# Kernel tuning notes

Measured on AMD Instinct MI355X. Metric: run time of the kernel, lower is better.

The kernel has to match this reference:

```python
import jax, jax.numpy as jnp
import numpy as np

N_HEAD = 12
HEAD_DIM = 64
EPS = 1e-6
ROPE_BASE = 10000.0


def rms_norm(x, w):
    x32 = x.astype(jnp.float32)
    var = jnp.mean(x32 * x32, axis=-1, keepdims=True)
    xn = x32 * jax.lax.rsqrt(var + EPS)
    return w * xn.astype(x.dtype)


def rotate_half(x):
    x1, x2 = jnp.split(x, 2, axis=-1)
    return jnp.concatenate((-x2, x1), axis=-1)


def rope_cos_sin(seq_len, dtype):
    inv_freq = 1.0 / (ROPE_BASE ** (jnp.arange(0, HEAD_DIM, 2, dtype=jnp.float32) / HEAD_DIM))
    pos = jnp.arange(seq_len, dtype=jnp.float32)
    freqs = pos[:, None] * inv_freq[None, :]          # [S, HEAD_DIM//2]
    emb = jnp.concatenate((freqs, freqs), axis=-1)    # [S, HEAD_DIM]
    # shape [1, 1, S, HEAD_DIM] (batch, head, seq, dim) after unsqueeze_dim=1
    return emb[None, None].astype(dtype), None  # placeholder, see below


def setup_inputs() -> dict:
    key = jax.random.key(0)
    ks = jax.random.split(key, 9)
    B, S, D, F = 1, 4096, 768, 2048
    s = 0.02
    return {
        "hidden_states": jax.random.normal(ks[0], (B, S, D), jnp.float32),
        "w_q": jax.random.normal(ks[1], (D, D), jnp.float32) * s,
        "w_k": jax.random.normal(ks[2], (D, D), jnp.float32) * s,
        "w_v": jax.random.normal(ks[3], (D, D), jnp.float32) * s,
        "w_o": jax.random.normal(ks[4], (D, D), jnp.float32) * s,
        "w_gate": jax.random.normal(ks[5], (D, F), jnp.float32) * s,
        "w_up": jax.random.normal(ks[6], (D, F), jnp.float32) * s,
        "w_down": jax.random.normal(ks[7], (F, D), jnp.float32) * s,
        "w_norm1": jnp.ones((D,), jnp.float32),
        "w_norm2": jnp.ones((D,), jnp.float32),
    }


def attention(x, w_q, w_k, w_v, w_o):
    B, S, D = x.shape
    scale = HEAD_DIM ** -0.5
    # project and split heads: [B, H, S, hd]
    q = (x @ w_q).reshape(B, S, N_HEAD, HEAD_DIM).transpose(0, 2, 1, 3)
    k = (x @ w_k).reshape(B, S, N_HEAD, HEAD_DIM).transpose(0, 2, 1, 3)
    v = (x @ w_v).reshape(B, S, N_HEAD, HEAD_DIM).transpose(0, 2, 1, 3)
    # rotary embedding (position_ids = arange(S))
    inv_freq = 1.0 / (ROPE_BASE ** (jnp.arange(0, HEAD_DIM, 2, dtype=jnp.float32) / HEAD_DIM))
    pos = jnp.arange(S, dtype=jnp.float32)
    freqs = pos[:, None] * inv_freq[None, :]
    emb = jnp.concatenate((freqs, freqs), axis=-1)          # [S, hd]
    cos = jnp.cos(emb).astype(x.dtype)[None, None]          # [1,1,S,hd]
    sin = jnp.sin(emb).astype(x.dtype)[None, None]
    q = q * cos + rotate_half(q) * sin
    k = k * cos + rotate_half(k) * sin
    # eager attention with causal mask (materialized, as in the original)
    scores = jnp.einsum("bhqd,bhkd->bhqk", q, k) * scale
    causal = jnp.triu(jnp.ones((S, S), dtype=bool), k=1)
    scores = jnp.where(causal, jnp.finfo(scores.dtype).min, scores)
    attn = jax.nn.softmax(scores.astype(jnp.float32), axis=-1).astype(q.dtype)
    out = jnp.einsum("bhqk,bhkd->bhqd", attn, v)
    out = out.transpose(0, 2, 1, 3).reshape(B, S, D)
    return out @ w_o


def reference(hidden_states, w_q, w_k, w_v, w_o, w_gate, w_up, w_down, w_norm1, w_norm2):
    x = hidden_states
    h = x + attention(rms_norm(x, w_norm1), w_q, w_k, w_v, w_o)
    y = rms_norm(h, w_norm2)
    ffn = (jax.nn.silu(y @ w_gate) * (y @ w_up)) @ w_down
    return h + ffn
```

## Files before the change

kernel.cpp:

```cpp
#include <hip/hip_runtime.h>
#include <hip/hip_bf16.h>

typedef __attribute__((ext_vector_type(8))) short s8v;
typedef __attribute__((ext_vector_type(4))) float f4v;
typedef __attribute__((ext_vector_type(16))) float f16v;
typedef __attribute__((ext_vector_type(4))) unsigned u4v;

typedef __attribute__((address_space(1))) const void as1_void;
typedef __attribute__((address_space(3))) void as3_void;

__device__ __forceinline__ void gl16(const void* g, void* l) {
  __builtin_amdgcn_global_load_lds((as1_void*)g, (as3_void*)l, 16, 0, 0);
}

__device__ __forceinline__ float b2f(int u) {
  union { float f; unsigned i; } c; c.i = ((unsigned)(u & 0xFFFF)) << 16; return c.f;
}
__device__ __forceinline__ unsigned short f2b(float f) {
  union { float f; unsigned i; } c; c.f = f;
  unsigned r = c.i + 0x7FFFu + ((c.i >> 16) & 1u);
  return (unsigned short)(r >> 16);
}
__device__ __forceinline__ unsigned pk2(float lo, float hi) {
  unsigned u;
  asm("v_cvt_pk_bf16_f32 %0, %1, %2" : "=v"(u) : "v"(lo), "v"(hi));
  return u;
}

#define MFMA16(a, b, c) __builtin_amdgcn_mfma_f32_16x16x32_bf16((a), (b), (c), 0, 0, 0)
#define MFMA32(a, b, c) __builtin_amdgcn_mfma_f32_32x32x16_bf16((a), (b), (c), 0, 0, 0)

__device__ __forceinline__ void xcd_remap(int nbn, int& bm, int& bn) {
  const int flat = blockIdx.x;
  const int u = (flat & 7) * ((int)gridDim.x >> 3) + (flat >> 3);
  bm = u / nbn;
  bn = u - bm * nbn;
}

struct Seg { const float* src; unsigned short* dst; int K; int N; int nbn; int nblocks; int mode; };
struct PrepArgs { Seg seg[9]; float* ct; float* st; const float* wn1; };

__global__ __launch_bounds__(256) void prep_k(PrepArgs a) {
  int b = blockIdx.x, si = 0;
  while (si < 8 && b >= a.seg[si].nblocks) { b -= a.seg[si].nblocks; ++si; }
  const Seg s = a.seg[si];
  const int tid = threadIdx.x;
  if (s.mode == 3) {
    const int t = b * 256 + tid;
    const int sq = t >> 5, d = t & 31;
    const float inv = powf(10000.0f, -(float)d * (1.0f / 32.0f));
    const float ang = (float)sq * inv;
    a.ct[t] = cosf(ang);
    a.st[t] = sinf(ang);
    return;
  }
  if (s.mode == 4) {
    const float* xr = s.src + (size_t)b * 768;
    float v0 = xr[tid], v1 = xr[tid + 256], v2 = xr[tid + 512];
    float ss = v0 * v0 + v1 * v1 + v2 * v2;
#pragma unroll
    for (int m = 1; m < 64; m <<= 1) ss += __shfl_xor(ss, m, 64);
    __shared__ float sred[4];
    if ((tid & 63) == 0) sred[tid >> 6] = ss;
    __syncthreads();
    const float tot = sred[0] + sred[1] + sred[2] + sred[3];
    const float rn = rsqrtf(tot * (1.0f / 768.0f) + 1e-6f);
    unsigned short* orow = s.dst + (size_t)b * 768;
    orow[tid]       = f2b(v0 * rn * a.wn1[tid]);
    orow[tid + 256] = f2b(v1 * rn * a.wn1[tid + 256]);
    orow[tid + 512] = f2b(v2 * rn * a.wn1[tid + 512]);
    return;
  }
  __shared__ float tile[32][33];
  const int tx = tid & 31, ty = tid >> 5;
  const int bn = b % s.nbn, bk = b / s.nbn;
#pragma unroll
  for (int i = 0; i < 32; i += 8)
    tile[ty + i][tx] = s.src[(size_t)(bk * 32 + ty + i) * s.N + bn * 32 + tx];
  __syncthreads();
#pragma unroll
  for (int i = 0; i < 32; i += 8) {
    int row;
    if (s.mode == 0)      row = bn * 32 + ty + i;
    else                  row = bn * 64 + (s.mode == 2 ? 32 : 0) + ty + i;
    s.dst[(size_t)row * s.K + bk * 32 + tx] = f2b(tile[tx][ty + i]);
  }
}

__global__ __launch_bounds__(256) void rmsnorm_k(const float* __restrict__ x,
    const float* __restrict__ w, unsigned short* __restrict__ out) {
  const int row = blockIdx.x, tid = threadIdx.x;
  const float* xr = x + (size_t)row * 768;
  float v0 = xr[tid], v1 = xr[tid + 256], v2 = xr[tid + 512];
  float ss = v0 * v0 + v1 * v1 + v2 * v2;
#pragma unroll
  for (int m = 1; m < 64; m <<= 1) ss += __shfl_xor(ss, m, 64);
  __shared__ float sred[4];
  if ((tid & 63) == 0) sred[tid >> 6] = ss;
  __syncthreads();
  const float tot = sred[0] + sred[1] + sred[2] + sred[3];
  const float rn = rsqrtf(tot * (1.0f / 768.0f) + 1e-6f);
  unsigned short* orow = out + (size_t)row * 768;
  orow[tid]       = f2b(v0 * rn * w[tid]);
  orow[tid + 256] = f2b(v1 * rn * w[tid + 256]);
  orow[tid + 512] = f2b(v2 * rn * w[tid + 512]);
}

template <int EPI, int BM, int BN>
__global__ __launch_bounds__(256) void gemm_bt(const unsigned short* __restrict__ A,
    const unsigned short* __restrict__ Bt, unsigned short* __restrict__ Cb,
    float* __restrict__ Cf, const float* __restrict__ R, int K, int ldc,
    const float* __restrict__ ct, const float* __restrict__ st, int nbn) {
  constexpr int ABYTES = BM * 32 * 2;
  constexpr int BBYTES = BN * 32 * 2;
  constexpr int APASS = BM / 64, BPASS = BN / 64;
  constexpr int LPS = APASS + BPASS;
  constexpr int MR = (BM == 128 && BN == 128) ? 4 : (BM == 128 ? 2 : 1);
  __shared__ unsigned short As[3 * BM * 32];
  __shared__ unsigned short Bs[3 * BN * 32];
  const int tid = threadIdx.x;
  const int lane = tid & 63, wid = tid >> 6;
  const int wrow = (BN == 128) ? (wid >> 1) * 64 : wid * (BM / 4);
  const int wcol = (BN == 128) ? (wid & 1) * 64 : 0;
  const int l15 = lane & 15, l4 = lane >> 4;
  int bm, bn;
  xcd_remap(nbn, bm, bn);

  f4v acc[MR][4] = {};

  const int o0 = tid * 16, o1 = tid * 16 + 4096;
  const int r0 = o0 >> 6, c0 = o0 & 63;
  const int r1 = o1 >> 6, c1 = o1 & 63;
  const size_t ldab = (size_t)K * 2;
  const char* Abyte = (const char*)A;
  const char* Bbyte = (const char*)Bt;
  const size_t a0 = (size_t)(bm * BM + r0) * ldab + c0;
  const size_t a1 = (size_t)(bm * BM + (APASS == 2 ? r1 : r0)) * ldab + c1;
  const size_t b0 = (size_t)(bn * BN + r0) * ldab + c0;
  const size_t b1 = (size_t)(bn * BN + (BPASS == 2 ? r1 : r0)) * ldab + c1;
  char* AsB = (char*)As;
  char* BsB = (char*)Bs;
  const int uoff = wid << 10;

#define STAGEK(I, SL) do { const size_t kb = (size_t)(I) * 64;                 \
    char* Aw = AsB + (SL) * ABYTES;                                            \
    char* Bw = BsB + (SL) * BBYTES;                                            \
    gl16(Abyte + a0 + kb, Aw + uoff);                                          \
    if constexpr (APASS == 2) gl16(Abyte + a1 + kb, Aw + uoff + 4096);         \
    gl16(Bbyte + b0 + kb, Bw + uoff);                                          \
    if constexpr (BPASS == 2) gl16(Bbyte + b1 + kb, Bw + uoff + 4096); } while (0)

  const int NI = K >> 5;
  STAGEK(0, 0);
  STAGEK(1, 1);
  int sel = 0, nsl = 2;

  for (int i = 0; i < NI; ++i) {
    if (i < NI - 1) {
      if constexpr (LPS == 4)      asm volatile("s_waitcnt vmcnt(4)" ::: "memory");
      else if constexpr (LPS == 3) asm volatile("s_waitcnt vmcnt(3)" ::: "memory");
      else                         asm volatile("s_waitcnt vmcnt(2)" ::: "memory");
    } else {
      asm volatile("s_waitcnt vmcnt(0)" ::: "memory");
    }
    __builtin_amdgcn_s_barrier();
    __builtin_amdgcn_sched_barrier(0);
    if (i + 2 < NI) STAGEK(i + 2, nsl);
    const char* Ar = AsB + sel * ABYTES;
    const char* Br = BsB + sel * BBYTES;
    s8v af[MR], bf[4];
#pragma unroll
    for (int m = 0; m < MR; ++m)
      af[m] = *(const s8v*)(Ar + (wrow + m * 16 + l15) * 64 + l4 * 16);
#pragma unroll
    for (int n = 0; n < 4; ++n)
      bf[n] = *(const s8v*)(Br + (wcol + n * 16 + l15) * 64 + l4 * 16);
    __builtin_amdgcn_s_setprio(1);
#pragma unroll
    for (int m = 0; m < MR; ++m)
#pragma unroll
      for (int n = 0; n < 4; ++n) acc[m][n] = MFMA16(af[m], bf[n], acc[m][n]);
    __builtin_amdgcn_s_setprio(0);
    sel = (sel == 2) ? 0 : sel + 1;
    nsl = (nsl == 2) ? 0 : nsl + 1;
  }
#undef STAGEK

  const int row0 = bm * BM + wrow;
  const int col0 = bn * BN + wcol;

  if constexpr (EPI == 2) {
    if (bn < 12) {
#pragma unroll
      for (int m = 0; m < MR; ++m)
#pragma unroll
        for (int r = 0; r < 4; ++r) {
          const int row = row0 + m * 16 + l4 * 4 + r;
#pragma unroll
          for (int n = 0; n < 2; ++n) {
            const int d = n * 16 + l15;
            const float c  = ct[row * 32 + d];
            const float sn = st[row * 32 + d];
            const float aa = acc[m][n][r], bb = acc[m][n + 2][r];
            acc[m][n][r]     = aa * c - bb * sn;
            acc[m][n + 2][r] = bb * c + aa * sn;
          }
        }
    }
    if (bn < 6) {
      const float QSC = 0.18033688011112042f;
#pragma unroll
      for (int m = 0; m < MR; ++m)
#pragma unroll
        for (int n = 0; n < 4; ++n)
#pragma unroll
          for (int r = 0; r < 4; ++r) acc[m][n][r] *= QSC;
    }
  }

#pragma unroll
  for (int m = 0; m < MR; ++m)
#pragma unroll
    for (int n = 0; n < 4; ++n)
#pragma unroll
      for (int r = 0; r < 4; ++r) {
        const int row = row0 + m * 16 + l4 * 4 + r;
        const int col = col0 + n * 16 + l15;
        const float v = acc[m][n][r];
        if (EPI == 1) {
          Cf[(size_t)row * ldc + col] = v + R[(size_t)row * ldc + col];
        } else {
          Cb[(size_t)row * ldc + col] = f2b(v);
        }
      }
}

template <int EPI>
__global__ __launch_bounds__(512, 2) void gemm_big(const unsigned short* __restrict__ A,
    const unsigned short* __restrict__ Bt, unsigned short* __restrict__ Cb,
    int K, int ldc, int nbn) {
  constexpr int ABYTES = 256 * 32 * 2;
  constexpr int BBYTES = 128 * 32 * 2;
  __shared__ unsigned short As[3 * 256 * 32];
  __shared__ unsigned short Bs[3 * 128 * 32];
  const int tid = threadIdx.x;
  const int lane = tid & 63, wid = tid >> 6;
  const int wm = wid >> 1, wn = wid & 1;
  const int wrow = wm * 64, wcol = wn * 64;
  const int l15 = lane & 15, l4 = lane >> 4;
  int bm, bn;
  xcd_remap(nbn, bm, bn);

  f4v acc[4][4] = {};

  const size_t ldab = (size_t)K * 2;
  const char* Ab = (const char*)A;
  const char* Bb = (const char*)Bt;
  const int lrow = lane >> 2, lch = (lane & 3) * 16;
  const size_t aS0 = (size_t)(bm * 256 + wid * 16 + lrow) * ldab + lch;
  const size_t aS1 = (size_t)(bm * 256 + (wid + 8) * 16 + lrow) * ldab + lch;
  const size_t bS  = (size_t)(bn * 128 + wid * 16 + lrow) * ldab + lch;
  char* AsB = (char*)As;
  char* BsB = (char*)Bs;
  const int uA0 = wid << 10, uA1 = (wid + 8) << 10, uB = wid << 10;

#define STAGEK(I, SL) do { const size_t kb = (size_t)(I) * 64;                 \
    gl16(Ab + aS0 + kb, AsB + (SL) * ABYTES + uA0);                            \
    gl16(Ab + aS1 + kb, AsB + (SL) * ABYTES + uA1);                            \
    gl16(Bb + bS  + kb, BsB + (SL) * BBYTES + uB); } while (0)

  const int NI = K >> 5;
  STAGEK(0, 0);
  STAGEK(1, 1);
  int sel = 0, nsl = 2;

  for (int i = 0; i < NI; ++i) {
    if (i < NI - 1) asm volatile("s_waitcnt vmcnt(3)" ::: "memory");
    else            asm volatile("s_waitcnt vmcnt(0)" ::: "memory");
    __builtin_amdgcn_s_barrier();
    __builtin_amdgcn_sched_barrier(0);
    if (i + 2 < NI) STAGEK(i + 2, nsl);
    const char* Ar = AsB + sel * ABYTES;
    const char* Br = BsB + sel * BBYTES;
    s8v af[4], bf[4];
#pragma unroll
    for (int m = 0; m < 4; ++m)
      af[m] = *(const s8v*)(Ar + (wrow + m * 16 + l15) * 64 + l4 * 16);
#pragma unroll
    for (int n = 0; n < 4; ++n)
      bf[n] = *(const s8v*)(Br + (wcol + n * 16 + l15) * 64 + l4 * 16);
    __builtin_amdgcn_s_setprio(1);
#pragma unroll
    for (int m = 0; m < 4; ++m)
#pragma unroll
      for (int n = 0; n < 4; ++n) acc[m][n] = MFMA16(af[m], bf[n], acc[m][n]);
    __builtin_amdgcn_s_setprio(0);
    sel = (sel == 2) ? 0 : sel + 1;
    nsl = (nsl == 2) ? 0 : nsl + 1;
  }
#undef STAGEK

  const int row0 = bm * 256 + wrow;
  const int col0 = bn * 128 + wcol;

  if (EPI == 3) {
    const int colb = (bn * 2 + wn) * 32;
#pragma unroll
    for (int m = 0; m < 4; ++m)
#pragma unroll
      for (int n = 0; n < 2; ++n)
#pragma unroll
        for (int r = 0; r < 4; ++r) {
          const int row = row0 + m * 16 + l4 * 4 + r;
          const float g = acc[m][n][r], u = acc[m][n + 2][r];
          const float val = g * u / (1.0f + __expf(-g));
          Cb[(size_t)row * 2048 + colb + n * 16 + l15] = f2b(val);
        }
    return;
  }

#pragma unroll
  for (int m = 0; m < 4; ++m)
#pragma unroll
    for (int n = 0; n < 4; ++n)
#pragma unroll
      for (int r = 0; r < 4; ++r) {
        const int row = row0 + m * 16 + l4 * 4 + r;
        const int col = col0 + n * 16 + l15;
        Cb[(size_t)row * ldc + col] = f2b(acc[m][n][r]);
      }
}

__global__ __launch_bounds__(256, 4) void flash_k(const unsigned short* __restrict__ qkv,
    uint2* __restrict__ Opart, float* __restrict__ ml) {
  const int kh = blockIdx.x, p = blockIdx.y, h = blockIdx.z;
  const int qbA = 63 - p;
  const int tid = threadIdx.x;
  const int wv = tid >> 6, lane = tid & 63;
  const int l31 = lane & 31, h8 = lane >> 5;
  const int myqb = (wv & 1) ? p : qbA;
  const int qrel = (wv >> 1) * 32 + l31;
  const int q_abs = myqb * 64 + qrel;

  __shared__ unsigned short Ks[2][64 * 72];
  __shared__ unsigned short Vt[2][64 * 72];

  const unsigned short* qp = qkv + h * 64;
  const unsigned short* kp = qkv + 768 + h * 64;
  const unsigned short* vp = qkv + 1536 + h * 64;

  s8v qf[4];
#pragma unroll
  for (int cc = 0; cc < 4; ++cc)
    qf[cc] = *(const s8v*)(qp + (size_t)q_abs * 2304 + cc * 16 + h8 * 8);

  f16v o0 = {}, o1 = {};
  float lp = 0.f;

  const int krow = tid >> 3, kc = (tid & 7) * 8;
  const int vj = tid & 31, vd0 = (tid >> 5) * 8;

  s8v ka, kb, va, vb;
#define LOADT(T) do { const size_t k0n = (size_t)(T) * 64;                    \
    ka = *(const s8v*)(kp + (k0n + krow) * 2304 + kc);                        \
    kb = *(const s8v*)(kp + (k0n + krow + 32) * 2304 + kc);                   \
    va = *(const s8v*)(vp + (k0n + 2 * vj) * 2304 + vd0);                     \
    vb = *(const s8v*)(vp + (k0n + 2 * vj + 1) * 2304 + vd0); } while (0)
#define WRITET(BUF) do {                                                      \
    *(s8v*)(Ks[BUF] + krow * 72 + kc) = ka;                                   \
    *(s8v*)(Ks[BUF] + (krow + 32) * 72 + kc) = kb;                            \
    unsigned* vtw = (unsigned*)(Vt[BUF] + (size_t)vd0 * 72 + 2 * vj);         \
    _Pragma("unroll")                                                         \
    for (int i = 0; i < 8; ++i)                                               \
      vtw[i * 36] = ((unsigned)(unsigned short)va[i]) |                       \
                    (((unsigned)(unsigned short)vb[i]) << 16); } while (0)

  LOADT(kh);
  WRITET(0);
  if (kh + 2 <= qbA) LOADT(kh + 2);
  __syncthreads();

  for (int t = kh; t <= qbA; t += 2) {
    const int cur = (t >> 1) & 1;
    if (t <= myqb) {
      f16v s0 = {}, s1 = {};
      __builtin_amdgcn_s_setprio(1);
#pragma unroll
      for (int cc = 0; cc < 4; ++cc) {
        const s8v kf0 = *(const s8v*)(Ks[cur] + l31 * 72 + cc * 16 + h8 * 8);
        const s8v kf1 = *(const s8v*)(Ks[cur] + (32 + l31) * 72 + cc * 16 + h8 * 8);
        s0 = MFMA32(kf0, qf[cc], s0);
        s1 = MFMA32(kf1, qf[cc], s1);
      }
      __builtin_amdgcn_s_setprio(0);
      if (t == myqb) {
#pragma unroll
        for (int rr = 0; rr < 16; ++rr) {
          const int koff = (rr & 3) + 8 * (rr >> 2) + 4 * h8;
          if (koff > qrel) s0[rr] = -1e30f;
          if (koff + 32 > qrel) s1[rr] = -1e30f;
        }
      }
#pragma unroll
      for (int rr = 0; rr < 16; ++rr) {
        s0[rr] = exp2f(s0[rr]);
        s1[rr] = exp2f(s1[rr]);
      }
      float sm[8];
#pragma unroll
      for (int i = 0; i < 8; ++i) sm[i] = (s0[i] + s0[i + 8]) + (s1[i] + s1[i + 8]);
#pragma unroll
      for (int i = 0; i < 4; ++i) sm[i] += sm[i + 4];
      lp += (sm[0] + sm[1]) + (sm[2] + sm[3]);

      unsigned pk0[8], pk1[8];
#pragma unroll
      for (int g = 0; g < 4; ++g)
#pragma unroll
        for (int j = 0; j < 2; ++j) {
          pk0[g * 2 + j] = pk2(s0[g * 4 + 2 * j], s0[g * 4 + 2 * j + 1]);
          pk1[g * 2 + j] = pk2(s1[g * 4 + 2 * j], s1[g * 4 + 2 * j + 1]);
        }
      __builtin_amdgcn_s_setprio(1);
#pragma unroll
      for (int cc = 0; cc < 4; ++cc) {
        const int g0 = (cc & 1) * 2, g1 = g0 + 1;
        const unsigned pA0 = (cc & 2) ? pk1[g0 * 2 + 0] : pk0[g0 * 2 + 0];
        const unsigned pA1 = (cc & 2) ? pk1[g0 * 2 + 1] : pk0[g0 * 2 + 1];
        const unsigned pB0 = (cc & 2) ? pk1[g1 * 2 + 0] : pk0[g1 * 2 + 0];
        const unsigned pB1 = (cc & 2) ? pk1[g1 * 2 + 1] : pk0[g1 * 2 + 1];
        const unsigned t00 = __shfl_xor((int)pA0, 32);
        const unsigned t01 = __shfl_xor((int)pA1, 32);
        const unsigned t10 = __shfl_xor((int)pB0, 32);
        const unsigned t11 = __shfl_xor((int)pB1, 32);
        union { u4v u; s8v s; } pf;
        pf.u[0] = h8 ? t10 : pA0;
        pf.u[1] = h8 ? t11 : pA1;
        pf.u[2] = h8 ? pB0 : t00;
        pf.u[3] = h8 ? pB1 : t01;
        const s8v vf0 = *(const s8v*)(Vt[cur] + l31 * 72 + cc * 16 + h8 * 8);
        const s8v vf1 = *(const s8v*)(Vt[cur] + (32 + l31) * 72 + cc * 16 + h8 * 8);
        o0 = MFMA32(vf0, pf.s, o0);
        o1 = MFMA32(vf1, pf.s, o1);
      }
      __builtin_amdgcn_s_setprio(0);
    }
    if (t + 2 <= qbA) {
      WRITET(cur ^ 1);
      if (t + 4 <= qbA) LOADT(t + 4);
      __syncthreads();
    }
  }

  lp += __shfl_xor(lp, 32);

  const size_t obase = ((size_t)kh * 12 + h) * 16 * 4096;
#pragma unroll
  for (int g = 0; g < 4; ++g) {
    const uint2 v0 = make_uint2(pk2(o0[g * 4], o0[g * 4 + 1]), pk2(o0[g * 4 + 2], o0[g * 4 + 3]));
    const uint2 v1 = make_uint2(pk2(o1[g * 4], o1[g * 4 + 1]), pk2(o1[g * 4 + 2], o1[g * 4 + 3]));
    Opart[obase + (size_t)(2 * g + h8) * 4096 + q_abs] = v0;
    Opart[obase + (size_t)(8 + 2 * g + h8) * 4096 + q_abs] = v1;
  }
  if (h8 == 0)
    ml[((size_t)kh * 12 + h) * 4096 + q_abs] = lp;
#undef LOADT
#undef WRITET
}

__global__ __launch_bounds__(256) void combine_k(const uint2* __restrict__ Opart,
    const float* __restrict__ ml, unsigned short* __restrict__ out) {
  const int u = blockIdx.x * 256 + threadIdx.x;
  const int q = u & 4095;
  const int rest = u >> 12;
  const int dgrp = rest & 15;
  const int h = rest >> 4;
  const float l0 = ml[h * 4096 + q];
  const float l1 = ml[12 * 4096 + h * 4096 + q];
  const float inv = 1.0f / (l0 + l1);
  const size_t idx = ((size_t)h * 16 + dgrp) * 4096 + q;
  const uint2 a = Opart[idx];
  const uint2 b = Opart[(size_t)12 * 16 * 4096 + idx];
  const int dbase = (dgrp < 8) ? 4 * dgrp : 32 + 4 * (dgrp - 8);
  ushort4 r;
  r.x = f2b((b2f(a.x) + b2f(b.x)) * inv);
  r.y = f2b((b2f(a.x >> 16) + b2f(b.x >> 16)) * inv);
  r.z = f2b((b2f(a.y) + b2f(b.y)) * inv);
  r.w = f2b((b2f(a.y >> 16) + b2f(b.y >> 16)) * inv);
  *(ushort4*)(out + (size_t)q * 768 + h * 64 + dbase) = r;
}

extern "C" void kernel_launch(void* const* d_in, const int* in_sizes, int n_in,
                              void* d_out, int out_size, void* d_ws, size_t ws_size,
                              hipStream_t stream) {
  const float* x    = (const float*)d_in[0];
  const float* w_q  = (const float*)d_in[1];
  const float* w_k  = (const float*)d_in[2];
  const float* w_v  = (const float*)d_in[3];
  const float* w_o  = (const float*)d_in[4];
  const float* w_g  = (const float*)d_in[5];
  const float* w_u  = (const float*)d_in[6];
  const float* w_d  = (const float*)d_in[7];
  const float* w_n1 = (const float*)d_in[8];
  const float* w_n2 = (const float*)d_in[9];
  (void)in_sizes; (void)n_in; (void)out_size; (void)ws_size;

  char* ws = (char*)d_ws;
  size_t off = 0;
  auto alloc = [&](size_t bytes) { char* p = ws + off; off += (bytes + 255) & ~(size_t)255; return p; };
  unsigned short* wqkvT = (unsigned short*)alloc(2304ull * 768 * 2);
  unsigned short* woT   = (unsigned short*)alloc(768ull * 768 * 2);
  unsigned short* wguT  = (unsigned short*)alloc(4096ull * 768 * 2);
  unsigned short* wdT   = (unsigned short*)alloc(768ull * 2048 * 2);
  float* ct             = (float*)alloc(4096ull * 32 * 4);
  float* st             = (float*)alloc(4096ull * 32 * 4);
  unsigned short* xn    = (unsigned short*)alloc(4096ull * 768 * 2);
  unsigned short* qkv   = (unsigned short*)alloc(4096ull * 2304 * 2);
  unsigned short* attn  = (unsigned short*)alloc(4096ull * 768 * 2);
  float* hbuf           = (float*)alloc(4096ull * 768 * 4);
  unsigned short* ybuf  = (unsigned short*)alloc(4096ull * 768 * 2);
  unsigned short* ffn   = (unsigned short*)alloc(4096ull * 2048 * 2);
  uint2* Opart          = (uint2*)alloc(2ull * 12 * 16 * 4096 * 8);
  float* mlb            = (float*)alloc(2ull * 12 * 4096 * 4);

  PrepArgs pa;
  pa.seg[0] = { w_q, wqkvT,                 768,  768, 24,  576, 0 };
  pa.seg[1] = { w_k, wqkvT + 768 * 768,     768,  768, 24,  576, 0 };
  pa.seg[2] = { w_v, wqkvT + 2 * 768 * 768, 768,  768, 24,  576, 0 };
  pa.seg[3] = { w_o, woT,                   768,  768, 24,  576, 0 };
  pa.seg[4] = { w_g, wguT,                  768, 2048, 64, 1536, 1 };
  pa.seg[5] = { w_u, wguT,                  768, 2048, 64, 1536, 2 };
  pa.seg[6] = { w_d, wdT,                  2048,  768, 24, 1536, 0 };
  pa.seg[7] = { nullptr, nullptr, 0, 0, 0, 512, 3 };
  pa.seg[8] = { x, xn, 0, 0, 0, 4096, 4 };
  pa.ct = ct; pa.st = st; pa.wn1 = w_n1;
  const int prep_blocks = 576 * 4 + 1536 * 3 + 512 + 4096;

  prep_k<<<prep_blocks, 256, 0, stream>>>(pa);
  gemm_bt<2, 128, 128><<<576, 256, 0, stream>>>(xn, wqkvT, qkv, nullptr, nullptr, 768, 2304, ct, st, 18);
  flash_k<<<dim3(2, 32, 12), 256, 0, stream>>>(qkv, Opart, mlb);
  combine_k<<<3072, 256, 0, stream>>>(Opart, mlb, attn);
  gemm_bt<1, 64, 64><<<768, 256, 0, stream>>>(attn, woT, nullptr, hbuf, x, 768, 768, nullptr, nullptr, 12);
  rmsnorm_k<<<4096, 256, 0, stream>>>(hbuf, w_n2, ybuf);
  gemm_big<3><<<512, 512, 0, stream>>>(ybuf, wguT, ffn, 768, 2048, 32);
  gemm_bt<1, 64, 64><<<768, 256, 0, stream>>>(ffn, wdT, nullptr, (float*)d_out, hbuf, 2048, 768, nullptr, nullptr, 12);
}
```

Measured before the change: 203.7 us.

## Store residual h in bf16 and shrink QKV GEMM tile to 64x128

The intermediate residual h is now stored as bf16 instead of fp32. The output-projection epilogue rounds it, the second RMSNorm reads bf16, and the down-projection epilogue adds the bf16 residual back. The QKV projection also switches from 128x128 to 64x128 tiles, doubling the grid for better CU occupancy, with the RoPE and scale gating rewritten in terms of column offsets. This cuts memory traffic on h but introduces bf16 rounding into the residual path, which could affect accuracy.

```diff
diff --git a/kernel.cpp b/kernel.cpp
--- a/kernel.cpp
+++ b/kernel.cpp
@@ -87,11 +87,11 @@
   }
 }
 
-__global__ __launch_bounds__(256) void rmsnorm_k(const float* __restrict__ x,
+__global__ __launch_bounds__(256) void rmsnorm_b16_k(const unsigned short* __restrict__ x,
     const float* __restrict__ w, unsigned short* __restrict__ out) {
   const int row = blockIdx.x, tid = threadIdx.x;
-  const float* xr = x + (size_t)row * 768;
-  float v0 = xr[tid], v1 = xr[tid + 256], v2 = xr[tid + 512];
+  const unsigned short* xr = x + (size_t)row * 768;
+  float v0 = b2f(xr[tid]), v1 = b2f(xr[tid + 256]), v2 = b2f(xr[tid + 512]);
   float ss = v0 * v0 + v1 * v1 + v2 * v2;
 #pragma unroll
   for (int m = 1; m < 64; m <<= 1) ss += __shfl_xor(ss, m, 64);
@@ -109,19 +109,20 @@
 template <int EPI, int BM, int BN>
 __global__ __launch_bounds__(256) void gemm_bt(const unsigned short* __restrict__ A,
     const unsigned short* __restrict__ Bt, unsigned short* __restrict__ Cb,
-    float* __restrict__ Cf, const float* __restrict__ R, int K, int ldc,
-    const float* __restrict__ ct, const float* __restrict__ st, int nbn) {
+    float* __restrict__ Cf, const float* __restrict__ Rf, const unsigned short* __restrict__ Rb,
+    int K, int ldc, const float* __restrict__ ct, const float* __restrict__ st, int nbn) {
   constexpr int ABYTES = BM * 32 * 2;
   constexpr int BBYTES = BN * 32 * 2;
   constexpr int APASS = BM / 64, BPASS = BN / 64;
   constexpr int LPS = APASS + BPASS;
-  constexpr int MR = (BM == 128 && BN == 128) ? 4 : (BM == 128 ? 2 : 1);
+  constexpr bool W2x2 = (BN == 128);
+  constexpr int MR = W2x2 ? (BM / 32) : (BM / 64);
   __shared__ unsigned short As[3 * BM * 32];
   __shared__ unsigned short Bs[3 * BN * 32];
   const int tid = threadIdx.x;
   const int lane = tid & 63, wid = tid >> 6;
-  const int wrow = (BN == 128) ? (wid >> 1) * 64 : wid * (BM / 4);
-  const int wcol = (BN == 128) ? (wid & 1) * 64 : 0;
+  const int wrow = W2x2 ? (wid >> 1) * (BM / 2) : wid * (BM / 4);
+  const int wcol = W2x2 ? (wid & 1) * 64 : 0;
   const int l15 = lane & 15, l4 = lane >> 4;
   int bm, bn;
   xcd_remap(nbn, bm, bn);
@@ -190,7 +191,8 @@
   const int col0 = bn * BN + wcol;
 
   if constexpr (EPI == 2) {
-    if (bn < 12) {
+    const int colw = col0;
+    if (colw < 1536) {
 #pragma unroll
       for (int m = 0; m < MR; ++m)
 #pragma unroll
@@ -207,7 +209,7 @@
           }
         }
     }
-    if (bn < 6) {
+    if (colw < 768) {
       const float QSC = 0.18033688011112042f;
 #pragma unroll
       for (int m = 0; m < MR; ++m)
@@ -227,11 +229,10 @@
         const int row = row0 + m * 16 + l4 * 4 + r;
         const int col = col0 + n * 16 + l15;
         const float v = acc[m][n][r];
-        if (EPI == 1) {
-          Cf[(size_t)row * ldc + col] = v + R[(size_t)row * ldc + col];
-        } else {
-          Cb[(size_t)row * ldc + col] = f2b(v);
-        }
+        const size_t idx = (size_t)row * ldc + col;
+        if (EPI == 4)      Cb[idx] = f2b(v + Rf[idx]);
+        else if (EPI == 5) Cf[idx] = v + b2f(Rb[idx]);
+        else               Cb[idx] = f2b(v);
       }
 }
 
@@ -517,7 +518,7 @@
   unsigned short* xn    = (unsigned short*)alloc(4096ull * 768 * 2);
   unsigned short* qkv   = (unsigned short*)alloc(4096ull * 2304 * 2);
   unsigned short* attn  = (unsigned short*)alloc(4096ull * 768 * 2);
-  float* hbuf           = (float*)alloc(4096ull * 768 * 4);
+  unsigned short* hb16  = (unsigned short*)alloc(4096ull * 768 * 2);
   unsigned short* ybuf  = (unsigned short*)alloc(4096ull * 768 * 2);
   unsigned short* ffn   = (unsigned short*)alloc(4096ull * 2048 * 2);
   uint2* Opart          = (uint2*)alloc(2ull * 12 * 16 * 4096 * 8);
@@ -537,11 +538,11 @@
   const int prep_blocks = 576 * 4 + 1536 * 3 + 512 + 4096;
 
   prep_k<<<prep_blocks, 256, 0, stream>>>(pa);
-  gemm_bt<2, 128, 128><<<576, 256, 0, stream>>>(xn, wqkvT, qkv, nullptr, nullptr, 768, 2304, ct, st, 18);
+  gemm_bt<2, 64, 128><<<1152, 256, 0, stream>>>(xn, wqkvT, qkv, nullptr, nullptr, nullptr, 768, 2304, ct, st, 18);
   flash_k<<<dim3(2, 32, 12), 256, 0, stream>>>(qkv, Opart, mlb);
   combine_k<<<3072, 256, 0, stream>>>(Opart, mlb, attn);
-  gemm_bt<1, 64, 64><<<768, 256, 0, stream>>>(attn, woT, nullptr, hbuf, x, 768, 768, nullptr, nullptr, 12);
-  rmsnorm_k<<<4096, 256, 0, stream>>>(hbuf, w_n2, ybuf);
+  gemm_bt<4, 64, 64><<<768, 256, 0, stream>>>(attn, woT, hb16, nullptr, x, nullptr, 768, 768, nullptr, nullptr, 12);
+  rmsnorm_b16_k<<<4096, 256, 0, stream>>>(hb16, w_n2, ybuf);
   gemm_big<3><<<512, 512, 0, stream>>>(ybuf, wguT, ffn, 768, 2048, 32);
-  gemm_bt<1, 64, 64><<<768, 256, 0, stream>>>(ffn, wdT, nullptr, (float*)d_out, hbuf, 2048, 768, nullptr, nullptr, 12);
-}
+  gemm_bt<5, 64, 64><<<768, 256, 0, stream>>>(ffn, wdT, nullptr, (float*)d_out, nullptr, hb16, 2048, 768, nullptr, nullptr, 12);
+}
```

New measurement: 212.5 us. 4.3% more time.
